# Kernel optimization log

Hardware: AMD Instinct MI355X
Metric: run time of the kernel (lower is better)

The kernel has to match this reference:

```python
import jax, jax.numpy as jnp
import numpy as np

D_MODEL = 1024
N_HEADS = 16
HEAD_DIM = D_MODEL // N_HEADS


def setup_inputs() -> dict:
    key = jax.random.key(0)
    ks = jax.random.split(key, 5)
    s_in = 1.0 / np.sqrt(D_MODEL)
    x = jax.random.normal(ks[0], (4, 2048, D_MODEL), dtype=jnp.float32)
    w_qkv = jax.random.uniform(ks[1], (3 * D_MODEL, D_MODEL), dtype=jnp.float32, minval=-s_in, maxval=s_in)
    b_qkv = jax.random.uniform(ks[2], (3 * D_MODEL,), dtype=jnp.float32, minval=-s_in, maxval=s_in)
    w_out = jax.random.uniform(ks[3], (D_MODEL, D_MODEL), dtype=jnp.float32, minval=-s_in, maxval=s_in)
    b_out = jax.random.uniform(ks[4], (D_MODEL,), dtype=jnp.float32, minval=-s_in, maxval=s_in)
    return {"x": x, "w_qkv": w_qkv, "b_qkv": b_qkv, "w_out": w_out, "b_out": b_out}


def reference(x, w_qkv, b_qkv, w_out, b_out):
    B, T, D = x.shape
    H, hd = N_HEADS, HEAD_DIM
    qkv = x @ w_qkv.T + b_qkv                      # [B, T, 3D]
    q, k, v = jnp.split(qkv, 3, axis=-1)
    # [B, H, T, hd]
    q = q.reshape(B, T, H, hd).transpose(0, 2, 1, 3)
    k = k.reshape(B, T, H, hd).transpose(0, 2, 1, 3)
    v = v.reshape(B, T, H, hd).transpose(0, 2, 1, 3)
    scale = 1.0 / np.sqrt(hd).astype(np.float32)
    attn = jnp.einsum('bhqd,bhkd->bhqk', q, k) * scale
    causal = jnp.triu(jnp.ones((T, T), dtype=bool), k=1)
    attn = jnp.where(causal, -jnp.inf, attn)
    attn = jax.nn.softmax(attn, axis=-1)
    out = jnp.einsum('bhqk,bhkd->bhqd', attn, v)
    out = out.transpose(0, 2, 1, 3).reshape(B, T, D)
    return out @ w_out.T + b_out
```

## Files before the change

kernel.cpp:

```cpp
#include <hip/hip_runtime.h>
#include <hip/hip_bf16.h>
#include <stdint.h>

#define D_MODEL 1024
#define NHEADS 16
#define HD 64
#define BB 4
#define TT 2048
#define MM (BB*TT)
#define NQKV (3*D_MODEL)
#define KK D_MODEL

typedef __attribute__((ext_vector_type(4))) float f32x4;
typedef __attribute__((ext_vector_type(8))) short bf16x8;

__device__ __forceinline__ unsigned short f2bf(float x){
    union { __hip_bfloat16 h; unsigned short u; } c;
    c.h = __float2bfloat16(x);
    return c.u;
}

__device__ __forceinline__ void gload_lds16(const void* g, void* l){
    __builtin_amdgcn_global_load_lds(
        (const __attribute__((address_space(1))) unsigned int*)g,
        (__attribute__((address_space(3))) unsigned int*)l,
        16, 0, 0);
}

#define N4_X  (MM*KK/4)
#define N4_WQ (NQKV*KK/4)
#define N4_WO (D_MODEL*D_MODEL/4)
__global__ void cast3_kernel(const float* __restrict__ x, const float* __restrict__ wq,
                             const float* __restrict__ wo,
                             unsigned short* __restrict__ xb, unsigned short* __restrict__ wqb,
                             unsigned short* __restrict__ wob){
    int i = blockIdx.x * blockDim.x + threadIdx.x;
    const float* src; unsigned short* dst; int j;
    if (i < N4_X)              { src = x;  dst = xb;  j = i; }
    else if (i < N4_X + N4_WQ) { src = wq; dst = wqb; j = i - N4_X; }
    else                       { src = wo; dst = wob; j = i - N4_X - N4_WQ; }
    float4 v = reinterpret_cast<const float4*>(src)[j];
    ushort4 o;
    o.x = f2bf(v.x); o.y = f2bf(v.y); o.z = f2bf(v.z); o.w = f2bf(v.w);
    reinterpret_cast<ushort4*>(dst)[j] = o;
}

__global__ __launch_bounds__(256) void gemm_qkv(
    const unsigned short* __restrict__ A, const unsigned short* __restrict__ Bw,
    const float* __restrict__ bias,
    unsigned short* __restrict__ qb, unsigned short* __restrict__ kb,
    unsigned short* __restrict__ vtb)
{
    __shared__ alignas(16) unsigned short As[2][128*32];
    __shared__ alignas(16) unsigned short Bs[2][128*32];
    const int tiles_n = NQKV/128;
    int nwg = gridDim.x;
    int orig = blockIdx.x;
    int bid = (orig & 7) * (nwg >> 3) + (orig >> 3);
    int bm = (bid / tiles_n) * 128;
    int bn = (bid % tiles_n) * 128;
    int tid = threadIdx.x;
    int w = tid >> 6, l = tid & 63;
    int wr = (w >> 1) * 64, wc = (w & 1) * 64;
    int lr = l & 15, hi = l >> 4;

    f32x4 acc[4][4] = {};

    int srow = tid >> 2;
    int scol = (tid & 3) * 8;
    const unsigned short* Ap = A + (size_t)(bm + srow) * KK + scol;
    const unsigned short* Bp = Bw + (size_t)(bn + srow) * KK + scol;

    {
        char* AsB = (char*)&As[0][0] + w*1024;
        char* BsB = (char*)&Bs[0][0] + w*1024;
        gload_lds16(Ap,           AsB);
        gload_lds16(Ap + 64*KK,   AsB + 4096);
        gload_lds16(Bp,           BsB);
        gload_lds16(Bp + 64*KK,   BsB + 4096);
    }
    __syncthreads();

    int cur = 0;
    for (int k0 = 0; k0 < KK; k0 += 32) {
        if (k0 + 32 < KK) {
            char* AsB = (cur ? (char*)&As[0][0] : (char*)&As[1][0]) + w*1024;
            char* BsB = (cur ? (char*)&Bs[0][0] : (char*)&Bs[1][0]) + w*1024;
            gload_lds16(Ap + k0 + 32,          AsB);
            gload_lds16(Ap + 64*KK + k0 + 32,  AsB + 4096);
            gload_lds16(Bp + k0 + 32,          BsB);
            gload_lds16(Bp + 64*KK + k0 + 32,  BsB + 4096);
        }
        const unsigned short* Ab = cur ? &As[1][0] : &As[0][0];
        const unsigned short* Bb = cur ? &Bs[1][0] : &Bs[0][0];
        bf16x8 af[4], bfr[4];
        #pragma unroll
        for (int m = 0; m < 4; m++)
            af[m] = *reinterpret_cast<const bf16x8*>(&Ab[(wr + m*16 + lr)*32 + hi*8]);
        #pragma unroll
        for (int n = 0; n < 4; n++)
            bfr[n] = *reinterpret_cast<const bf16x8*>(&Bb[(wc + n*16 + lr)*32 + hi*8]);
        #pragma unroll
        for (int m = 0; m < 4; m++)
            #pragma unroll
            for (int n = 0; n < 4; n++)
                acc[m][n] = __builtin_amdgcn_mfma_f32_16x16x32_bf16(af[m], bfr[n], acc[m][n], 0, 0, 0);
        __syncthreads();
        cur ^= 1;
    }

    #pragma unroll
    for (int m = 0; m < 4; m++) {
        int gm = bm + wr + m*16 + hi*4;
        int b  = gm >> 11;
        int t  = gm & 2047;
        #pragma unroll
        for (int n = 0; n < 4; n++) {
            int gn = bn + wc + n*16 + lr;
            float bv = bias[gn];
            int sec = gn >> 10;
            int nn  = gn & 1023;
            int h = nn >> 6, d = nn & 63;
            int bh = b * NHEADS + h;
            if (sec == 2) {
                ushort4 pk;
                pk.x = f2bf(acc[m][n][0] + bv);
                pk.y = f2bf(acc[m][n][1] + bv);
                pk.z = f2bf(acc[m][n][2] + bv);
                pk.w = f2bf(acc[m][n][3] + bv);
                *reinterpret_cast<ushort4*>(&vtb[((size_t)bh*HD + d)*TT + t]) = pk;
            } else {
                unsigned short* dst = (sec == 0) ? qb : kb;
                #pragma unroll
                for (int r = 0; r < 4; r++)
                    dst[((size_t)bh*TT + t + r)*HD + d] = f2bf(acc[m][n][r] + bv);
            }
        }
    }
}

__global__ __launch_bounds__(512) void attn_kernel(
    const unsigned short* __restrict__ qb, const unsigned short* __restrict__ kb,
    const unsigned short* __restrict__ vtb, unsigned short* __restrict__ ao)
{
    __shared__ alignas(16) unsigned short Kt[4][64*64];
    __shared__ alignas(16) unsigned short Vt[4][64*64];
    __shared__ alignas(16) unsigned short Pl[8][16*64];

    const int bh = blockIdx.x;
    const int qt = (gridDim.y - 1) - blockIdx.y;
    const int tid = threadIdx.x;
    const int w = tid >> 6, l = tid & 63;
    const int lr = l & 15, hi = l >> 4;

    const int qbase = qt * 128;
    const int qrow  = qbase + w*16;
    const int npairs = qt + 1;

    const unsigned short* Qp = qb + ((size_t)bh*TT + qrow) * HD;
    bf16x8 qf0 = *reinterpret_cast<const bf16x8*>(Qp + lr*HD + hi*8);
    bf16x8 qf1 = *reinterpret_cast<const bf16x8*>(Qp + lr*HD + 32 + hi*8);

    const unsigned short* Kg = kb  + (size_t)bh*TT*HD;
    const unsigned short* Vg = vtb + (size_t)bh*HD*TT;

    const int srow = w*8 + (l >> 3);
    const int sc16 = (l & 7) ^ (srow & 7);
    char* KS0 = (char*)&Kt[0][0] + w*1024;  char* KS1 = (char*)&Kt[1][0] + w*1024;
    char* KS2 = (char*)&Kt[2][0] + w*1024;  char* KS3 = (char*)&Kt[3][0] + w*1024;
    char* VS0 = (char*)&Vt[0][0] + w*1024;  char* VS1 = (char*)&Vt[1][0] + w*1024;
    char* VS2 = (char*)&Vt[2][0] + w*1024;  char* VS3 = (char*)&Vt[3][0] + w*1024;

    gload_lds16(Kg + (size_t)srow*HD + sc16*8,        KS0);
    gload_lds16(Vg + (size_t)srow*TT + sc16*8,        VS0);
    gload_lds16(Kg + (size_t)(64 + srow)*HD + sc16*8, KS1);
    gload_lds16(Vg + (size_t)srow*TT + 64 + sc16*8,   VS1);
    __syncthreads();

    float mS = -3e38f, lS = 0.f;
    f32x4 o[4] = {};
    const float sc = 0.125f * 1.4426950408889634f;
    const float THR = 8.0f / sc;
    const int qg = qrow + lr;
    const int swp = (lr & 7) << 4;
    char* Pw = (char*)&Pl[w][0];

    for (int j = 0; j < npairs; ++j) {
        const int ph = j & 1;
        const char* Ka = ph ? (const char*)&Kt[2][0] : (const char*)&Kt[0][0];
        const char* Kc = ph ? (const char*)&Kt[3][0] : (const char*)&Kt[1][0];
        const char* Va = ph ? (const char*)&Vt[2][0] : (const char*)&Vt[0][0];
        const char* Vc = ph ? (const char*)&Vt[3][0] : (const char*)&Vt[1][0];
        if (j + 1 < npairs) {
            const int tn = 2*j + 2;
            char* kd0 = ph ? KS0 : KS2;  char* kd1 = ph ? KS1 : KS3;
            char* vd0 = ph ? VS0 : VS2;  char* vd1 = ph ? VS1 : VS3;
            gload_lds16(Kg + (size_t)(tn*64 + srow)*HD + sc16*8,      kd0);
            gload_lds16(Vg + (size_t)srow*TT + tn*64 + sc16*8,        vd0);
            gload_lds16(Kg + (size_t)(tn*64 + 64 + srow)*HD + sc16*8, kd1);
            gload_lds16(Vg + (size_t)srow*TT + tn*64 + 64 + sc16*8,   vd1);
        }
        const int kba = 2*j*64;
        const int kbb = kba + 64;
        const bool cb = (kbb <= qrow + 15);

        f32x4 sa4[4] = {}, sb4[4] = {};
        __builtin_amdgcn_s_setprio(1);
        #pragma unroll
        for (int n = 0; n < 4; n++) {
            int rb = (n*16 + lr) * 128;
            bf16x8 k0 = *reinterpret_cast<const bf16x8*>(Ka + rb + (( 0 + hi*16) ^ swp));
            bf16x8 k1 = *reinterpret_cast<const bf16x8*>(Ka + rb + ((64 + hi*16) ^ swp));
            sa4[n] = __builtin_amdgcn_mfma_f32_16x16x32_bf16(k0, qf0, sa4[n], 0, 0, 0);
            sa4[n] = __builtin_amdgcn_mfma_f32_16x16x32_bf16(k1, qf1, sa4[n], 0, 0, 0);
        }
        if (cb) {
            #pragma unroll
            for (int n = 0; n < 4; n++) {
                int rb = (n*16 + lr) * 128;
                bf16x8 k0 = *reinterpret_cast<const bf16x8*>(Kc + rb + (( 0 + hi*16) ^ swp));
                bf16x8 k1 = *reinterpret_cast<const bf16x8*>(Kc + rb + ((64 + hi*16) ^ swp));
                sb4[n] = __builtin_amdgcn_mfma_f32_16x16x32_bf16(k0, qf0, sb4[n], 0, 0, 0);
                sb4[n] = __builtin_amdgcn_mfma_f32_16x16x32_bf16(k1, qf1, sb4[n], 0, 0, 0);
            }
        }
        __builtin_amdgcn_s_setprio(0);

        if (kba + 63 > qrow) {
            #pragma unroll
            for (int n = 0; n < 4; n++)
                #pragma unroll
                for (int r = 0; r < 4; r++)
                    if (kba + n*16 + hi*4 + r > qg) sa4[n][r] = -3e38f;
        }
        if (cb && kbb + 63 > qrow) {
            #pragma unroll
            for (int n = 0; n < 4; n++)
                #pragma unroll
                for (int r = 0; r < 4; r++)
                    if (kbb + n*16 + hi*4 + r > qg) sb4[n][r] = -3e38f;
        }

        float t0 = fmaxf(fmaxf(sa4[0][0], sa4[0][1]), fmaxf(sa4[0][2], sa4[0][3]));
        float t1 = fmaxf(fmaxf(sa4[1][0], sa4[1][1]), fmaxf(sa4[1][2], sa4[1][3]));
        float t2 = fmaxf(fmaxf(sa4[2][0], sa4[2][1]), fmaxf(sa4[2][2], sa4[2][3]));
        float t3 = fmaxf(fmaxf(sa4[3][0], sa4[3][1]), fmaxf(sa4[3][2], sa4[3][3]));
        float rm = fmaxf(fmaxf(t0, t1), fmaxf(t2, t3));
        if (cb) {
            float u0 = fmaxf(fmaxf(sb4[0][0], sb4[0][1]), fmaxf(sb4[0][2], sb4[0][3]));
            float u1 = fmaxf(fmaxf(sb4[1][0], sb4[1][1]), fmaxf(sb4[1][2], sb4[1][3]));
            float u2 = fmaxf(fmaxf(sb4[2][0], sb4[2][1]), fmaxf(sb4[2][2], sb4[2][3]));
            float u3 = fmaxf(fmaxf(sb4[3][0], sb4[3][1]), fmaxf(sb4[3][2], sb4[3][3]));
            rm = fmaxf(rm, fmaxf(fmaxf(u0, u1), fmaxf(u2, u3)));
        }
        rm = fmaxf(rm, __shfl_xor(rm, 16, 64));
        rm = fmaxf(rm, __shfl_xor(rm, 32, 64));
        if (!__all(rm - mS <= THR)) {
            float newm = fmaxf(mS, rm);
            float al = exp2f(sc * (mS - newm));
            mS = newm;
            lS *= al;
            #pragma unroll
            for (int r = 0; r < 4; r++) {
                float alr = __shfl(al, hi*4 + r, 64);
                o[0][r] *= alr; o[1][r] *= alr; o[2][r] *= alr; o[3][r] *= alr;
            }
        }
        const float c0 = sc * mS;

        float rs = 0.f;
        #pragma unroll
        for (int n = 0; n < 4; n++) {
            float p0 = exp2f(fmaf(sa4[n][0], sc, -c0));
            float p1 = exp2f(fmaf(sa4[n][1], sc, -c0));
            float p2 = exp2f(fmaf(sa4[n][2], sc, -c0));
            float p3 = exp2f(fmaf(sa4[n][3], sc, -c0));
            rs += (p0 + p1) + (p2 + p3);
            ushort4 u;
            u.x = f2bf(p0); u.y = f2bf(p1); u.z = f2bf(p2); u.w = f2bf(p3);
            *reinterpret_cast<ushort4*>(Pw + (lr*128 + ((n*32 + hi*8) ^ swp))) = u;
        }
        ushort4 ub[4];
        if (cb) {
            #pragma unroll
            for (int n = 0; n < 4; n++) {
                float p0 = exp2f(fmaf(sb4[n][0], sc, -c0));
                float p1 = exp2f(fmaf(sb4[n][1], sc, -c0));
                float p2 = exp2f(fmaf(sb4[n][2], sc, -c0));
                float p3 = exp2f(fmaf(sb4[n][3], sc, -c0));
                rs += (p0 + p1) + (p2 + p3);
                ub[n].x = f2bf(p0); ub[n].y = f2bf(p1);
                ub[n].z = f2bf(p2); ub[n].w = f2bf(p3);
            }
        }
        rs += __shfl_xor(rs, 16, 64);
        rs += __shfl_xor(rs, 32, 64);
        lS += rs;

        {
            bf16x8 pa0 = *reinterpret_cast<const bf16x8*>(Pw + (lr*128 + (( 0 + hi*16) ^ swp)));
            bf16x8 pa1 = *reinterpret_cast<const bf16x8*>(Pw + (lr*128 + ((64 + hi*16) ^ swp)));
            __builtin_amdgcn_s_setprio(1);
            #pragma unroll
            for (int nd = 0; nd < 4; nd++) {
                int rb = (nd*16 + lr) * 128;
                bf16x8 v0 = *reinterpret_cast<const bf16x8*>(Va + rb + (( 0 + hi*16) ^ swp));
                bf16x8 v1 = *reinterpret_cast<const bf16x8*>(Va + rb + ((64 + hi*16) ^ swp));
                o[nd] = __builtin_amdgcn_mfma_f32_16x16x32_bf16(pa0, v0, o[nd], 0, 0, 0);
                o[nd] = __builtin_amdgcn_mfma_f32_16x16x32_bf16(pa1, v1, o[nd], 0, 0, 0);
            }
            __builtin_amdgcn_s_setprio(0);
        }
        if (cb) {
            #pragma unroll
            for (int n = 0; n < 4; n++)
                *reinterpret_cast<ushort4*>(Pw + (lr*128 + ((n*32 + hi*8) ^ swp))) = ub[n];
            bf16x8 pa0 = *reinterpret_cast<const bf16x8*>(Pw + (lr*128 + (( 0 + hi*16) ^ swp)));
            bf16x8 pa1 = *reinterpret_cast<const bf16x8*>(Pw + (lr*128 + ((64 + hi*16) ^ swp)));
            __builtin_amdgcn_s_setprio(1);
            #pragma unroll
            for (int nd = 0; nd < 4; nd++) {
                int rb = (nd*16 + lr) * 128;
                bf16x8 v0 = *reinterpret_cast<const bf16x8*>(Vc + rb + (( 0 + hi*16) ^ swp));
                bf16x8 v1 = *reinterpret_cast<const bf16x8*>(Vc + rb + ((64 + hi*16) ^ swp));
                o[nd] = __builtin_amdgcn_mfma_f32_16x16x32_bf16(pa0, v0, o[nd], 0, 0, 0);
                o[nd] = __builtin_amdgcn_mfma_f32_16x16x32_bf16(pa1, v1, o[nd], 0, 0, 0);
            }
            __builtin_amdgcn_s_setprio(0);
        }
        __syncthreads();
    }

    float inv = 1.0f / lS;
    int b = bh >> 4, h = bh & 15;
    #pragma unroll
    for (int r = 0; r < 4; r++) {
        float invr = __shfl(inv, hi*4 + r, 64);
        int t = qrow + hi*4 + r;
        #pragma unroll
        for (int nd = 0; nd < 4; nd++) {
            float val = o[nd][r] * invr;
            ao[((size_t)b*TT + t)*D_MODEL + h*HD + nd*16 + lr] = f2bf(val);
        }
    }
}

__global__ __launch_bounds__(256) void gemm_out(
    const unsigned short* __restrict__ A, const unsigned short* __restrict__ Bw,
    const float* __restrict__ bias, float* __restrict__ out)
{
    __shared__ alignas(16) unsigned short As[2][128*32];
    __shared__ alignas(16) unsigned short Bs[2][128*32];
    const int tiles_n = D_MODEL/128;
    int nwg = gridDim.x;
    int orig = blockIdx.x;
    int bid = (orig & 7) * (nwg >> 3) + (orig >> 3);
    int bm = (bid / tiles_n) * 128;
    int bn = (bid % tiles_n) * 128;
    int tid = threadIdx.x;
    int w = tid >> 6, l = tid & 63;
    int wr = (w >> 1) * 64, wc = (w & 1) * 64;
    int lr = l & 15, hi = l >> 4;

    f32x4 acc[4][4] = {};

    int srow = tid >> 2;
    int scol = (tid & 3) * 8;
    const unsigned short* Ap = A + (size_t)(bm + srow) * KK + scol;
    const unsigned short* Bp = Bw + (size_t)(bn + srow) * KK + scol;

    {
        char* AsB = (char*)&As[0][0] + w*1024;
        char* BsB = (char*)&Bs[0][0] + w*1024;
        gload_lds16(Ap,           AsB);
        gload_lds16(Ap + 64*KK,   AsB + 4096);
        gload_lds16(Bp,           BsB);
        gload_lds16(Bp + 64*KK,   BsB + 4096);
    }
    __syncthreads();

    int cur = 0;
    for (int k0 = 0; k0 < KK; k0 += 32) {
        if (k0 + 32 < KK) {
            char* AsB = (cur ? (char*)&As[0][0] : (char*)&As[1][0]) + w*1024;
            char* BsB = (cur ? (char*)&Bs[0][0] : (char*)&Bs[1][0]) + w*1024;
            gload_lds16(Ap + k0 + 32,          AsB);
            gload_lds16(Ap + 64*KK + k0 + 32,  AsB + 4096);
            gload_lds16(Bp + k0 + 32,          BsB);
            gload_lds16(Bp + 64*KK + k0 + 32,  BsB + 4096);
        }
        const unsigned short* Ab = cur ? &As[1][0] : &As[0][0];
        const unsigned short* Bb = cur ? &Bs[1][0] : &Bs[0][0];
        bf16x8 af[4], bfr[4];
        #pragma unroll
        for (int m = 0; m < 4; m++)
            af[m] = *reinterpret_cast<const bf16x8*>(&Ab[(wr + m*16 + lr)*32 + hi*8]);
        #pragma unroll
        for (int n = 0; n < 4; n++)
            bfr[n] = *reinterpret_cast<const bf16x8*>(&Bb[(wc + n*16 + lr)*32 + hi*8]);
        #pragma unroll
        for (int m = 0; m < 4; m++)
            #pragma unroll
            for (int n = 0; n < 4; n++)
                acc[m][n] = __builtin_amdgcn_mfma_f32_16x16x32_bf16(af[m], bfr[n], acc[m][n], 0, 0, 0);
        __syncthreads();
        cur ^= 1;
    }

    #pragma unroll
    for (int m = 0; m < 4; m++) {
        int gm = bm + wr + m*16 + hi*4;
        #pragma unroll
        for (int n = 0; n < 4; n++) {
            int gn = bn + wc + n*16 + lr;
            float bv = bias[gn];
            #pragma unroll
            for (int r = 0; r < 4; r++)
                out[(size_t)(gm + r)*D_MODEL + gn] = acc[m][n][r] + bv;
        }
    }
}

extern "C" void kernel_launch(void* const* d_in, const int* in_sizes, int n_in,
                              void* d_out, int out_size, void* d_ws, size_t ws_size,
                              hipStream_t stream) {
    const float* x     = (const float*)d_in[0];
    const float* w_qkv = (const float*)d_in[1];
    const float* b_qkv = (const float*)d_in[2];
    const float* w_out = (const float*)d_in[3];
    const float* b_out = (const float*)d_in[4];
    float* out = (float*)d_out;

    char* ws = (char*)d_ws;
    unsigned short* xbf   = (unsigned short*)(ws);
    unsigned short* wqkvb = (unsigned short*)(ws + (size_t)16777216);
    unsigned short* woutb = (unsigned short*)(ws + (size_t)23068672);
    unsigned short* qb    = (unsigned short*)(ws + (size_t)25165824);
    unsigned short* kb    = (unsigned short*)(ws + (size_t)41943040);
    unsigned short* vtb   = (unsigned short*)(ws + (size_t)58720256);
    unsigned short* aob   = xbf;

    cast3_kernel<<<(N4_X + N4_WQ + N4_WO)/256, 256, 0, stream>>>(x, w_qkv, w_out, xbf, wqkvb, woutb);

    gemm_qkv<<<(MM/128)*(NQKV/128), 256, 0, stream>>>(xbf, wqkvb, b_qkv, qb, kb, vtb);
    attn_kernel<<<dim3(BB*NHEADS, TT/128), 512, 0, stream>>>(qb, kb, vtb, aob);
    gemm_out<<<(MM/128)*(D_MODEL/128), 256, 0, stream>>>(aob, woutb, b_out, out);
}
```

Baseline: 177.9 us.

## Rework GEMMs with 256x128 tiles, triple-buffered LDS and swizzled loads

Both the QKV and output-projection GEMMs now use 512-thread blocks with 256x128 tiles, a three-stage LDS ring filled by direct global-to-LDS loads, and explicit vmcnt waits with a single barrier per k-step. The LDS column index is XOR-swizzled to reduce bank conflicts, and MFMA issue is given raised wave priority. The goal is to hide global latency better and raise arithmetic intensity per block. In exchange it uses more LDS and registers per block, and the hand-written wait counts make correctness depend on exact load ordering.

After: 166.7 us. 1.07x faster.

```diff
diff --git a/kernel.cpp b/kernel.cpp
--- a/kernel.cpp
+++ b/kernel.cpp
@@ -45,78 +45,89 @@
     reinterpret_cast<ushort4*>(dst)[j] = o;
 }
 
-__global__ __launch_bounds__(256) void gemm_qkv(
+
+#define GEMM_PROLOGUE(A_, B_)                                                   \
+    const int tid = threadIdx.x;                                                \
+    const int w = tid >> 6, l = tid & 63;                                       \
+    const int wm = w >> 2, wn = w & 3;                                          \
+    const int lr = l & 15, hi = l >> 4;                                         \
+    f32x4 acc[8][2] = {};                                                       \
+    const int c16 = hi ^ (lr & 3);                                              \
+    const int base_a = (wm*128 + lr)*32 + c16*8;                                \
+    const int base_b = (wn*32  + lr)*32 + c16*8;                                \
+    const int g16 = ((tid & 3) ^ ((tid >> 2) & 3)) * 8;                         \
+    const unsigned short* Aap = A_ + (size_t)(bm + (tid >> 2)) * KK + g16;      \
+    const unsigned short* Bbp = B_ + (size_t)(bn + (tid >> 2)) * KK + g16;      \
+    char* AsL = (char*)&As[0][0];                                               \
+    char* BsL = (char*)&Bs[0][0];                                               \
+                      \
+    gload_lds16(Aap,                 AsL + tid*16);                             \
+    gload_lds16(Aap + 128*KK,        AsL + 8192 + tid*16);                      \
+    gload_lds16(Bbp,                 BsL + tid*16);                             \
+    gload_lds16(Aap + 32,            AsL + 16384 + tid*16);                     \
+    gload_lds16(Aap + 128*KK + 32,   AsL + 16384 + 8192 + tid*16);              \
+    gload_lds16(Bbp + 32,            BsL + 8192 + tid*16);
+
+#define GPHASE(VM, bc, bi, tnext, DOISSUE) do {                                 \
+    asm volatile("s_waitcnt vmcnt(" #VM ")" ::: "memory");                      \
+    __builtin_amdgcn_s_barrier();                                               \
+    asm volatile("" ::: "memory");                                              \
+    bf16x8 af[8], bfn[2];                                                       \
+    _Pragma("unroll")                                                           \
+    for (int m = 0; m < 8; m++)                                                 \
+        af[m] = *reinterpret_cast<const bf16x8*>(&As[bc][base_a + m*512]);      \
+    _Pragma("unroll")                                                           \
+    for (int n = 0; n < 2; n++)                                                 \
+        bfn[n] = *reinterpret_cast<const bf16x8*>(&Bs[bc][base_b + n*512]);     \
+    if (DOISSUE) {                                                              \
+        gload_lds16(Aap + (tnext)*32,           AsL + (bi)*16384 + tid*16);     \
+        gload_lds16(Aap + 128*KK + (tnext)*32,  AsL + (bi)*16384 + 8192 + tid*16);\
+        gload_lds16(Bbp + (tnext)*32,           BsL + (bi)*8192 + tid*16);      \
+    }                                                                           \
+    __builtin_amdgcn_s_setprio(1);                                              \
+    _Pragma("unroll")                                                           \
+    for (int m = 0; m < 8; m++) {                                               \
+        acc[m][0] = __builtin_amdgcn_mfma_f32_16x16x32_bf16(af[m], bfn[0], acc[m][0], 0, 0, 0); \
+        acc[m][1] = __builtin_amdgcn_mfma_f32_16x16x32_bf16(af[m], bfn[1], acc[m][1], 0, 0, 0); \
+    }                                                                           \
+    __builtin_amdgcn_s_setprio(0);                                              \
+} while(0)
+
+#define GEMM_MAINLOOP()                                                         \
+    for (int t3 = 0; t3 < 30; t3 += 3) {                                        \
+        GPHASE(3, 0, 2, t3+2, 1);                                               \
+        GPHASE(3, 1, 0, t3+3, 1);                                               \
+        GPHASE(3, 2, 1, t3+4, 1);                                               \
+    }                                                                           \
+    GPHASE(3, 0, 2, 0, 0);                                                      \
+    GPHASE(0, 1, 2, 0, 0);
+
+__global__ __launch_bounds__(512, 4) void gemm_qkv(
     const unsigned short* __restrict__ A, const unsigned short* __restrict__ Bw,
     const float* __restrict__ bias,
     unsigned short* __restrict__ qb, unsigned short* __restrict__ kb,
     unsigned short* __restrict__ vtb)
 {
-    __shared__ alignas(16) unsigned short As[2][128*32];
-    __shared__ alignas(16) unsigned short Bs[2][128*32];
+    __shared__ alignas(16) unsigned short As[3][256*32];
+    __shared__ alignas(16) unsigned short Bs[3][128*32];
     const int tiles_n = NQKV/128;
     int nwg = gridDim.x;
     int orig = blockIdx.x;
     int bid = (orig & 7) * (nwg >> 3) + (orig >> 3);
-    int bm = (bid / tiles_n) * 128;
+    int bm = (bid / tiles_n) * 256;
     int bn = (bid % tiles_n) * 128;
-    int tid = threadIdx.x;
-    int w = tid >> 6, l = tid & 63;
-    int wr = (w >> 1) * 64, wc = (w & 1) * 64;
-    int lr = l & 15, hi = l >> 4;
-
-    f32x4 acc[4][4] = {};
-
-    int srow = tid >> 2;
-    int scol = (tid & 3) * 8;
-    const unsigned short* Ap = A + (size_t)(bm + srow) * KK + scol;
-    const unsigned short* Bp = Bw + (size_t)(bn + srow) * KK + scol;
-
-    {
-        char* AsB = (char*)&As[0][0] + w*1024;
-        char* BsB = (char*)&Bs[0][0] + w*1024;
-        gload_lds16(Ap,           AsB);
-        gload_lds16(Ap + 64*KK,   AsB + 4096);
-        gload_lds16(Bp,           BsB);
-        gload_lds16(Bp + 64*KK,   BsB + 4096);
-    }
-    __syncthreads();
-
-    int cur = 0;
-    for (int k0 = 0; k0 < KK; k0 += 32) {
-        if (k0 + 32 < KK) {
-            char* AsB = (cur ? (char*)&As[0][0] : (char*)&As[1][0]) + w*1024;
-            char* BsB = (cur ? (char*)&Bs[0][0] : (char*)&Bs[1][0]) + w*1024;
-            gload_lds16(Ap + k0 + 32,          AsB);
-            gload_lds16(Ap + 64*KK + k0 + 32,  AsB + 4096);
-            gload_lds16(Bp + k0 + 32,          BsB);
-            gload_lds16(Bp + 64*KK + k0 + 32,  BsB + 4096);
-        }
-        const unsigned short* Ab = cur ? &As[1][0] : &As[0][0];
-        const unsigned short* Bb = cur ? &Bs[1][0] : &Bs[0][0];
-        bf16x8 af[4], bfr[4];
-        #pragma unroll
-        for (int m = 0; m < 4; m++)
-            af[m] = *reinterpret_cast<const bf16x8*>(&Ab[(wr + m*16 + lr)*32 + hi*8]);
-        #pragma unroll
-        for (int n = 0; n < 4; n++)
-            bfr[n] = *reinterpret_cast<const bf16x8*>(&Bb[(wc + n*16 + lr)*32 + hi*8]);
-        #pragma unroll
-        for (int m = 0; m < 4; m++)
-            #pragma unroll
-            for (int n = 0; n < 4; n++)
-                acc[m][n] = __builtin_amdgcn_mfma_f32_16x16x32_bf16(af[m], bfr[n], acc[m][n], 0, 0, 0);
-        __syncthreads();
-        cur ^= 1;
-    }
+
+    GEMM_PROLOGUE(A, Bw)
+    GEMM_MAINLOOP()
 
     #pragma unroll
-    for (int m = 0; m < 4; m++) {
-        int gm = bm + wr + m*16 + hi*4;
+    for (int m = 0; m < 8; m++) {
+        int gm = bm + wm*128 + m*16 + hi*4;
         int b  = gm >> 11;
         int t  = gm & 2047;
         #pragma unroll
-        for (int n = 0; n < 4; n++) {
-            int gn = bn + wc + n*16 + lr;
+        for (int n = 0; n < 2; n++) {
+            int gn = bn + wn*32 + n*16 + lr;
             float bv = bias[gn];
             int sec = gn >> 10;
             int nn  = gn & 1023;
@@ -139,6 +150,36 @@
     }
 }
 
+__global__ __launch_bounds__(512, 4) void gemm_out(
+    const unsigned short* __restrict__ A, const unsigned short* __restrict__ Bw,
+    const float* __restrict__ bias, float* __restrict__ out)
+{
+    __shared__ alignas(16) unsigned short As[3][256*32];
+    __shared__ alignas(16) unsigned short Bs[3][128*32];
+    const int tiles_n = D_MODEL/128;
+    int nwg = gridDim.x;
+    int orig = blockIdx.x;
+    int bid = (orig & 7) * (nwg >> 3) + (orig >> 3);
+    int bm = (bid / tiles_n) * 256;
+    int bn = (bid % tiles_n) * 128;
+
+    GEMM_PROLOGUE(A, Bw)
+    GEMM_MAINLOOP()
+
+    #pragma unroll
+    for (int m = 0; m < 8; m++) {
+        int gm = bm + wm*128 + m*16 + hi*4;
+        #pragma unroll
+        for (int n = 0; n < 2; n++) {
+            int gn = bn + wn*32 + n*16 + lr;
+            float bv = bias[gn];
+            #pragma unroll
+            for (int r = 0; r < 4; r++)
+                out[(size_t)(gm + r)*D_MODEL + gn] = acc[m][n][r] + bv;
+        }
+    }
+}
+
 __global__ __launch_bounds__(512) void attn_kernel(
     const unsigned short* __restrict__ qb, const unsigned short* __restrict__ kb,
     const unsigned short* __restrict__ vtb, unsigned short* __restrict__ ao)
@@ -345,82 +386,6 @@
     }
 }
 
-__global__ __launch_bounds__(256) void gemm_out(
-    const unsigned short* __restrict__ A, const unsigned short* __restrict__ Bw,
-    const float* __restrict__ bias, float* __restrict__ out)
-{
-    __shared__ alignas(16) unsigned short As[2][128*32];
-    __shared__ alignas(16) unsigned short Bs[2][128*32];
-    const int tiles_n = D_MODEL/128;
-    int nwg = gridDim.x;
-    int orig = blockIdx.x;
-    int bid = (orig & 7) * (nwg >> 3) + (orig >> 3);
-    int bm = (bid / tiles_n) * 128;
-    int bn = (bid % tiles_n) * 128;
-    int tid = threadIdx.x;
-    int w = tid >> 6, l = tid & 63;
-    int wr = (w >> 1) * 64, wc = (w & 1) * 64;
-    int lr = l & 15, hi = l >> 4;
-
-    f32x4 acc[4][4] = {};
-
-    int srow = tid >> 2;
-    int scol = (tid & 3) * 8;
-    const unsigned short* Ap = A + (size_t)(bm + srow) * KK + scol;
-    const unsigned short* Bp = Bw + (size_t)(bn + srow) * KK + scol;
-
-    {
-        char* AsB = (char*)&As[0][0] + w*1024;
-        char* BsB = (char*)&Bs[0][0] + w*1024;
-        gload_lds16(Ap,           AsB);
-        gload_lds16(Ap + 64*KK,   AsB + 4096);
-        gload_lds16(Bp,           BsB);
-        gload_lds16(Bp + 64*KK,   BsB + 4096);
-    }
-    __syncthreads();
-
-    int cur = 0;
-    for (int k0 = 0; k0 < KK; k0 += 32) {
-        if (k0 + 32 < KK) {
-            char* AsB = (cur ? (char*)&As[0][0] : (char*)&As[1][0]) + w*1024;
-            char* BsB = (cur ? (char*)&Bs[0][0] : (char*)&Bs[1][0]) + w*1024;
-            gload_lds16(Ap + k0 + 32,          AsB);
-            gload_lds16(Ap + 64*KK + k0 + 32,  AsB + 4096);
-            gload_lds16(Bp + k0 + 32,          BsB);
-            gload_lds16(Bp + 64*KK + k0 + 32,  BsB + 4096);
-        }
-        const unsigned short* Ab = cur ? &As[1][0] : &As[0][0];
-        const unsigned short* Bb = cur ? &Bs[1][0] : &Bs[0][0];
-        bf16x8 af[4], bfr[4];
-        #pragma unroll
-        for (int m = 0; m < 4; m++)
-            af[m] = *reinterpret_cast<const bf16x8*>(&Ab[(wr + m*16 + lr)*32 + hi*8]);
-        #pragma unroll
-        for (int n = 0; n < 4; n++)
-            bfr[n] = *reinterpret_cast<const bf16x8*>(&Bb[(wc + n*16 + lr)*32 + hi*8]);
-        #pragma unroll
-        for (int m = 0; m < 4; m++)
-            #pragma unroll
-            for (int n = 0; n < 4; n++)
-                acc[m][n] = __builtin_amdgcn_mfma_f32_16x16x32_bf16(af[m], bfr[n], acc[m][n], 0, 0, 0);
-        __syncthreads();
-        cur ^= 1;
-    }
-
-    #pragma unroll
-    for (int m = 0; m < 4; m++) {
-        int gm = bm + wr + m*16 + hi*4;
-        #pragma unroll
-        for (int n = 0; n < 4; n++) {
-            int gn = bn + wc + n*16 + lr;
-            float bv = bias[gn];
-            #pragma unroll
-            for (int r = 0; r < 4; r++)
-                out[(size_t)(gm + r)*D_MODEL + gn] = acc[m][n][r] + bv;
-        }
-    }
-}
-
 extern "C" void kernel_launch(void* const* d_in, const int* in_sizes, int n_in,
                               void* d_out, int out_size, void* d_ws, size_t ws_size,
                               hipStream_t stream) {
@@ -442,7 +407,7 @@
 
     cast3_kernel<<<(N4_X + N4_WQ + N4_WO)/256, 256, 0, stream>>>(x, w_qkv, w_out, xbf, wqkvb, woutb);
 
-    gemm_qkv<<<(MM/128)*(NQKV/128), 256, 0, stream>>>(xbf, wqkvb, b_qkv, qb, kb, vtb);
+    gemm_qkv<<<(MM/256)*(NQKV/128), 512, 0, stream>>>(xbf, wqkvb, b_qkv, qb, kb, vtb);
     attn_kernel<<<dim3(BB*NHEADS, TT/128), 512, 0, stream>>>(qb, kb, vtb, aob);
-    gemm_out<<<(MM/128)*(D_MODEL/128), 256, 0, stream>>>(aob, woutb, b_out, out);
-}
+    gemm_out<<<(MM/256)*(D_MODEL/128), 512, 0, stream>>>(aob, woutb, b_out, out);
+}
```

## Rewrite both GEMMs with 128x256 tiles, triple-buffered LDS, and XOR swizzle

Applied to the files above, without the earlier changes.

Replaces the two double-buffered 128x128 GEMM kernels with a shared core that uses 512-thread blocks, 128x256 tiles with K-step 64, and a three-stage LDS ring. It waits on vmcnt so loads stay two stages ahead, and interleaves global-to-LDS issues with MFMA phases under s_setprio. An XOR swizzle on the LDS layout is meant to avoid bank conflicts. LDS use grows to about 144KB per block, which limits occupancy, and the added barriers cost some synchronisation overhead.

New measurement: 186.8 us. +5.0%, slower.

```diff
diff --git a/kernel.cpp b/kernel.cpp
--- a/kernel.cpp
+++ b/kernel.cpp
@@ -45,78 +45,111 @@
     reinterpret_cast<ushort4*>(dst)[j] = o;
 }
 
-__global__ __launch_bounds__(256) void gemm_qkv(
+__device__ __forceinline__ void gemm_core(
+    const unsigned short* __restrict__ A_, const unsigned short* __restrict__ B_,
+    int bm, int bn, char* AsL, char* BsL, f32x4 (&acc)[4][4], int tid)
+{
+    const int w = tid >> 6, l = tid & 63;
+    const int wm = w >> 2, wn = w & 3;
+    const int lr = l & 15, hi = l >> 4;
+
+    const int swz = ((tid & 7) ^ ((tid >> 3) & 7)) * 8;
+    const unsigned short* Ag = A_ + (size_t)(bm + (tid >> 3)) * KK + swz;
+    const unsigned short* Bg = B_ + (size_t)(bn + (tid >> 3)) * KK + swz;
+
+    const int rowA = (wm*64 + lr) * 128;
+    const int rowB = (wn*64 + lr) * 128;
+    const int ck0 = ((0 + hi) ^ (lr & 7)) * 16;
+    const int ck1 = ((4 + hi) ^ (lr & 7)) * 16;
+
+    #pragma unroll
+    for (int tt = 0; tt < 2; tt++) {
+        const size_t k0 = (size_t)tt * 64;
+        gload_lds16(Ag + k0,                   AsL + tt*16384 + tid*16);
+        gload_lds16(Ag + (size_t)64*KK + k0,   AsL + tt*16384 + 8192 + tid*16);
+        #pragma unroll
+        for (int j = 0; j < 4; j++)
+            gload_lds16(Bg + (size_t)j*64*KK + k0, BsL + tt*32768 + j*8192 + tid*16);
+    }
+
+    bf16x8 bfr[4][2];
+    for (int t = 0; t < 16; ++t) {
+        const int c  = t % 3;
+        const int bi = (t + 2) % 3;
+        const bool doissue = (t < 14);
+        const size_t k2 = (size_t)(t + 2) * 64;
+        if (t < 15) asm volatile("s_waitcnt vmcnt(6)" ::: "memory");
+        else        asm volatile("s_waitcnt vmcnt(0)" ::: "memory");
+        __builtin_amdgcn_s_barrier();
+        const char* Ac = AsL + c*16384;
+        const char* Bc = BsL + c*32768;
+        #pragma unroll
+        for (int p = 0; p < 4; p++) {
+            bf16x8 a0 = *reinterpret_cast<const bf16x8*>(Ac + rowA + p*2048 + ck0);
+            bf16x8 a1 = *reinterpret_cast<const bf16x8*>(Ac + rowA + p*2048 + ck1);
+            if (p == 0) {
+                #pragma unroll
+                for (int n = 0; n < 4; n++) {
+                    bfr[n][0] = *reinterpret_cast<const bf16x8*>(Bc + rowB + n*2048 + ck0);
+                    bfr[n][1] = *reinterpret_cast<const bf16x8*>(Bc + rowB + n*2048 + ck1);
+                }
+            }
+            if (doissue) {
+                if (p == 0) {
+                    gload_lds16(Ag + k2,                 AsL + bi*16384 + tid*16);
+                    gload_lds16(Ag + (size_t)64*KK + k2, AsL + bi*16384 + 8192 + tid*16);
+                } else if (p == 1) {
+                    gload_lds16(Bg + k2,                  BsL + bi*32768 + tid*16);
+                    gload_lds16(Bg + (size_t)64*KK + k2,  BsL + bi*32768 + 8192 + tid*16);
+                } else if (p == 2) {
+                    gload_lds16(Bg + (size_t)128*KK + k2, BsL + bi*32768 + 16384 + tid*16);
+                    gload_lds16(Bg + (size_t)192*KK + k2, BsL + bi*32768 + 24576 + tid*16);
+                }
+            }
+            __builtin_amdgcn_s_barrier();
+            __builtin_amdgcn_s_setprio(1);
+            #pragma unroll
+            for (int n = 0; n < 4; n++)
+                acc[p][n] = __builtin_amdgcn_mfma_f32_16x16x32_bf16(a0, bfr[n][0], acc[p][n], 0, 0, 0);
+            #pragma unroll
+            for (int n = 0; n < 4; n++)
+                acc[p][n] = __builtin_amdgcn_mfma_f32_16x16x32_bf16(a1, bfr[n][1], acc[p][n], 0, 0, 0);
+            __builtin_amdgcn_s_setprio(0);
+            __builtin_amdgcn_s_barrier();
+        }
+    }
+}
+
+__global__ __launch_bounds__(512, 2) void gemm_qkv(
     const unsigned short* __restrict__ A, const unsigned short* __restrict__ Bw,
     const float* __restrict__ bias,
     unsigned short* __restrict__ qb, unsigned short* __restrict__ kb,
     unsigned short* __restrict__ vtb)
 {
-    __shared__ alignas(16) unsigned short As[2][128*32];
-    __shared__ alignas(16) unsigned short Bs[2][128*32];
-    const int tiles_n = NQKV/128;
+    __shared__ alignas(16) unsigned short As[3][128*64];
+    __shared__ alignas(16) unsigned short Bs[3][256*64];
+    const int tiles_n = NQKV/256;
     int nwg = gridDim.x;
     int orig = blockIdx.x;
     int bid = (orig & 7) * (nwg >> 3) + (orig >> 3);
     int bm = (bid / tiles_n) * 128;
-    int bn = (bid % tiles_n) * 128;
-    int tid = threadIdx.x;
-    int w = tid >> 6, l = tid & 63;
-    int wr = (w >> 1) * 64, wc = (w & 1) * 64;
-    int lr = l & 15, hi = l >> 4;
+    int bn = (bid % tiles_n) * 256;
 
     f32x4 acc[4][4] = {};
-
-    int srow = tid >> 2;
-    int scol = (tid & 3) * 8;
-    const unsigned short* Ap = A + (size_t)(bm + srow) * KK + scol;
-    const unsigned short* Bp = Bw + (size_t)(bn + srow) * KK + scol;
-
-    {
-        char* AsB = (char*)&As[0][0] + w*1024;
-        char* BsB = (char*)&Bs[0][0] + w*1024;
-        gload_lds16(Ap,           AsB);
-        gload_lds16(Ap + 64*KK,   AsB + 4096);
-        gload_lds16(Bp,           BsB);
-        gload_lds16(Bp + 64*KK,   BsB + 4096);
-    }
-    __syncthreads();
-
-    int cur = 0;
-    for (int k0 = 0; k0 < KK; k0 += 32) {
-        if (k0 + 32 < KK) {
-            char* AsB = (cur ? (char*)&As[0][0] : (char*)&As[1][0]) + w*1024;
-            char* BsB = (cur ? (char*)&Bs[0][0] : (char*)&Bs[1][0]) + w*1024;
-            gload_lds16(Ap + k0 + 32,          AsB);
-            gload_lds16(Ap + 64*KK + k0 + 32,  AsB + 4096);
-            gload_lds16(Bp + k0 + 32,          BsB);
-            gload_lds16(Bp + 64*KK + k0 + 32,  BsB + 4096);
-        }
-        const unsigned short* Ab = cur ? &As[1][0] : &As[0][0];
-        const unsigned short* Bb = cur ? &Bs[1][0] : &Bs[0][0];
-        bf16x8 af[4], bfr[4];
-        #pragma unroll
-        for (int m = 0; m < 4; m++)
-            af[m] = *reinterpret_cast<const bf16x8*>(&Ab[(wr + m*16 + lr)*32 + hi*8]);
-        #pragma unroll
-        for (int n = 0; n < 4; n++)
-            bfr[n] = *reinterpret_cast<const bf16x8*>(&Bb[(wc + n*16 + lr)*32 + hi*8]);
-        #pragma unroll
-        for (int m = 0; m < 4; m++)
-            #pragma unroll
-            for (int n = 0; n < 4; n++)
-                acc[m][n] = __builtin_amdgcn_mfma_f32_16x16x32_bf16(af[m], bfr[n], acc[m][n], 0, 0, 0);
-        __syncthreads();
-        cur ^= 1;
-    }
-
+    gemm_core(A, Bw, bm, bn, (char*)&As[0][0], (char*)&Bs[0][0], acc, threadIdx.x);
+
+    const int tid = threadIdx.x;
+    const int w = tid >> 6, l = tid & 63;
+    const int wm = w >> 2, wn = w & 3;
+    const int lr = l & 15, hi = l >> 4;
     #pragma unroll
     for (int m = 0; m < 4; m++) {
-        int gm = bm + wr + m*16 + hi*4;
+        int gm = bm + wm*64 + m*16 + hi*4;
         int b  = gm >> 11;
         int t  = gm & 2047;
         #pragma unroll
         for (int n = 0; n < 4; n++) {
-            int gn = bn + wc + n*16 + lr;
+            int gn = bn + wn*64 + n*16 + lr;
             float bv = bias[gn];
             int sec = gn >> 10;
             int nn  = gn & 1023;
@@ -139,6 +172,40 @@
     }
 }
 
+__global__ __launch_bounds__(512, 2) void gemm_out(
+    const unsigned short* __restrict__ A, const unsigned short* __restrict__ Bw,
+    const float* __restrict__ bias, float* __restrict__ out)
+{
+    __shared__ alignas(16) unsigned short As[3][128*64];
+    __shared__ alignas(16) unsigned short Bs[3][256*64];
+    const int tiles_n = D_MODEL/256;
+    int nwg = gridDim.x;
+    int orig = blockIdx.x;
+    int bid = (orig & 7) * (nwg >> 3) + (orig >> 3);
+    int bm = (bid / tiles_n) * 128;
+    int bn = (bid % tiles_n) * 256;
+
+    f32x4 acc[4][4] = {};
+    gemm_core(A, Bw, bm, bn, (char*)&As[0][0], (char*)&Bs[0][0], acc, threadIdx.x);
+
+    const int tid = threadIdx.x;
+    const int w = tid >> 6, l = tid & 63;
+    const int wm = w >> 2, wn = w & 3;
+    const int lr = l & 15, hi = l >> 4;
+    #pragma unroll
+    for (int m = 0; m < 4; m++) {
+        int gm = bm + wm*64 + m*16 + hi*4;
+        #pragma unroll
+        for (int n = 0; n < 4; n++) {
+            int gn = bn + wn*64 + n*16 + lr;
+            float bv = bias[gn];
+            #pragma unroll
+            for (int r = 0; r < 4; r++)
+                out[(size_t)(gm + r)*D_MODEL + gn] = acc[m][n][r] + bv;
+        }
+    }
+}
+
 __global__ __launch_bounds__(512) void attn_kernel(
     const unsigned short* __restrict__ qb, const unsigned short* __restrict__ kb,
     const unsigned short* __restrict__ vtb, unsigned short* __restrict__ ao)
@@ -345,82 +412,6 @@
     }
 }
 
-__global__ __launch_bounds__(256) void gemm_out(
-    const unsigned short* __restrict__ A, const unsigned short* __restrict__ Bw,
-    const float* __restrict__ bias, float* __restrict__ out)
-{
-    __shared__ alignas(16) unsigned short As[2][128*32];
-    __shared__ alignas(16) unsigned short Bs[2][128*32];
-    const int tiles_n = D_MODEL/128;
-    int nwg = gridDim.x;
-    int orig = blockIdx.x;
-    int bid = (orig & 7) * (nwg >> 3) + (orig >> 3);
-    int bm = (bid / tiles_n) * 128;
-    int bn = (bid % tiles_n) * 128;
-    int tid = threadIdx.x;
-    int w = tid >> 6, l = tid & 63;
-    int wr = (w >> 1) * 64, wc = (w & 1) * 64;
-    int lr = l & 15, hi = l >> 4;
-
-    f32x4 acc[4][4] = {};
-
-    int srow = tid >> 2;
-    int scol = (tid & 3) * 8;
-    const unsigned short* Ap = A + (size_t)(bm + srow) * KK + scol;
-    const unsigned short* Bp = Bw + (size_t)(bn + srow) * KK + scol;
-
-    {
-        char* AsB = (char*)&As[0][0] + w*1024;
-        char* BsB = (char*)&Bs[0][0] + w*1024;
-        gload_lds16(Ap,           AsB);
-        gload_lds16(Ap + 64*KK,   AsB + 4096);
-        gload_lds16(Bp,           BsB);
-        gload_lds16(Bp + 64*KK,   BsB + 4096);
-    }
-    __syncthreads();
-
-    int cur = 0;
-    for (int k0 = 0; k0 < KK; k0 += 32) {
-        if (k0 + 32 < KK) {
-            char* AsB = (cur ? (char*)&As[0][0] : (char*)&As[1][0]) + w*1024;
-            char* BsB = (cur ? (char*)&Bs[0][0] : (char*)&Bs[1][0]) + w*1024;
-            gload_lds16(Ap + k0 + 32,          AsB);
-            gload_lds16(Ap + 64*KK + k0 + 32,  AsB + 4096);
-            gload_lds16(Bp + k0 + 32,          BsB);
-            gload_lds16(Bp + 64*KK + k0 + 32,  BsB + 4096);
-        }
-        const unsigned short* Ab = cur ? &As[1][0] : &As[0][0];
-        const unsigned short* Bb = cur ? &Bs[1][0] : &Bs[0][0];
-        bf16x8 af[4], bfr[4];
-        #pragma unroll
-        for (int m = 0; m < 4; m++)
-            af[m] = *reinterpret_cast<const bf16x8*>(&Ab[(wr + m*16 + lr)*32 + hi*8]);
-        #pragma unroll
-        for (int n = 0; n < 4; n++)
-            bfr[n] = *reinterpret_cast<const bf16x8*>(&Bb[(wc + n*16 + lr)*32 + hi*8]);
-        #pragma unroll
-        for (int m = 0; m < 4; m++)
-            #pragma unroll
-            for (int n = 0; n < 4; n++)
-                acc[m][n] = __builtin_amdgcn_mfma_f32_16x16x32_bf16(af[m], bfr[n], acc[m][n], 0, 0, 0);
-        __syncthreads();
-        cur ^= 1;
-    }
-
-    #pragma unroll
-    for (int m = 0; m < 4; m++) {
-        int gm = bm + wr + m*16 + hi*4;
-        #pragma unroll
-        for (int n = 0; n < 4; n++) {
-            int gn = bn + wc + n*16 + lr;
-            float bv = bias[gn];
-            #pragma unroll
-            for (int r = 0; r < 4; r++)
-                out[(size_t)(gm + r)*D_MODEL + gn] = acc[m][n][r] + bv;
-        }
-    }
-}
-
 extern "C" void kernel_launch(void* const* d_in, const int* in_sizes, int n_in,
                               void* d_out, int out_size, void* d_ws, size_t ws_size,
                               hipStream_t stream) {
@@ -442,7 +433,7 @@
 
     cast3_kernel<<<(N4_X + N4_WQ + N4_WO)/256, 256, 0, stream>>>(x, w_qkv, w_out, xbf, wqkvb, woutb);
 
-    gemm_qkv<<<(MM/128)*(NQKV/128), 256, 0, stream>>>(xbf, wqkvb, b_qkv, qb, kb, vtb);
+    gemm_qkv<<<(MM/128)*(NQKV/256), 512, 0, stream>>>(xbf, wqkvb, b_qkv, qb, kb, vtb);
     attn_kernel<<<dim3(BB*NHEADS, TT/128), 512, 0, stream>>>(qb, kb, vtb, aob);
-    gemm_out<<<(MM/128)*(D_MODEL/128), 256, 0, stream>>>(aob, woutb, b_out, out);
-}
+    gemm_out<<<(MM/128)*(D_MODEL/256), 512, 0, stream>>>(aob, woutb, b_out, out);
+}
```
